# Kernel tuning notes

Measured on AMD Instinct MI355X. Metric: run time of the kernel, lower is better.

Reference implementation:

```python
import jax, jax.numpy as jnp
import numpy as np

B, N, E, D = 32, 512, 2048, 128
N_STEPS = 3


def setup_inputs() -> dict:
    key = jax.random.key(0)
    ks = jax.random.split(key, 16)
    s = 0.05
    return {
        "prop_state": jax.random.normal(ks[0], (B, N, D), jnp.float32),
        "edge_states": jax.random.normal(ks[1], (B, E, D), jnp.float32),
        "A": jax.random.uniform(ks[2], (B, N, E), jnp.float32) / E,
        "tem_features": jax.random.normal(ks[3], (B, 64), jnp.float32),
        "link_W": jax.random.normal(ks[4], (D, D), jnp.float32) * s,
        "link_b": jnp.zeros((D,), jnp.float32),
        "reset_W": jax.random.normal(ks[5], (2 * D, D), jnp.float32) * s,
        "reset_b": jnp.zeros((D,), jnp.float32),
        "update_W": jax.random.normal(ks[6], (2 * D, D), jnp.float32) * s,
        "update_b": jnp.zeros((D,), jnp.float32),
        "trans_W": jax.random.normal(ks[7], (2 * D, D), jnp.float32) * s,
        "trans_b": jnp.zeros((D,), jnp.float32),
        "att_W1": jax.random.normal(ks[8], (D, D), jnp.float32) * s,
        "att_b1": jnp.zeros((D,), jnp.float32),
        "att_W2": jax.random.normal(ks[9], (D, 1), jnp.float32) * s,
        "att_b2": jnp.zeros((1,), jnp.float32),
        "out_W": jax.random.normal(ks[10], (D, D), jnp.float32) * s,
        "out_b": jnp.zeros((D,), jnp.float32),
    }


def reference(prop_state, edge_states, A, tem_features,
              link_W, link_b, reset_W, reset_b, update_W, update_b,
              trans_W, trans_b, att_W1, att_b1, att_W2, att_b2, out_W, out_b):
    init_node = prop_state
    init_edge = edge_states
    for _ in range(N_STEPS):
        edge_states = edge_states @ link_W + link_b              # [B,E,D]
        a_cur = jnp.einsum('bne,bed->bnd', A, edge_states)       # [B,N,D]
        a = jnp.concatenate([a_cur, prop_state], axis=2)         # [B,N,2D]
        r = jax.nn.sigmoid(a @ reset_W + reset_b)
        z = jax.nn.sigmoid(a @ update_W + update_b)
        joined = jnp.concatenate([a_cur, r * prop_state], axis=2)
        h_hat = jnp.tanh(joined @ trans_W + trans_b)
        prop_state = (1.0 - z) * prop_state + z * h_hat
    # attention pooling
    atten = jnp.tanh(prop_state @ att_W1 + att_b1) @ att_W2 + att_b2   # [B,N,1]
    Aw = jax.nn.softmax(jnp.transpose(atten, (0, 2, 1)), axis=2)       # [B,1,N]
    out = jnp.tanh(prop_state @ out_W + out_b)                         # [B,N,D]
    mul = jnp.einsum('bqn,bnd->bqd', Aw, out)                          # [B,1,D]
    graph_out = jnp.tanh(jnp.squeeze(mul, axis=1))                     # [B,D]
    # residual block: mean over concatenated node+edge initial states
    feat = jnp.concatenate([init_node, init_edge], axis=1)             # [B,N+E,D]
    residual = jnp.mean(feat, axis=1)                                  # [B,D]
    res = jax.nn.relu(graph_out + residual)
    return res, mul, edge_states
```

## Files before the change

kernel.cpp:

```cpp
#include <hip/hip_runtime.h>
#include <hip/hip_bf16.h>


typedef unsigned short u16;
typedef __attribute__((ext_vector_type(4))) float f32x4;
typedef __attribute__((ext_vector_type(8))) short bf16x8;

#define DI static __device__ __forceinline__

DI u16 f2bf(float f) {
    unsigned u = __builtin_bit_cast(unsigned, f);
    return (u16)((u + 0x7fffu + ((u >> 16) & 1u)) >> 16);
}

DI bf16x8 cvt8(float4 a, float4 b) {
    u16 tmp[8] = {f2bf(a.x), f2bf(a.y), f2bf(a.z), f2bf(a.w),
                  f2bf(b.x), f2bf(b.y), f2bf(b.z), f2bf(b.w)};
    return *(const bf16x8*)tmp;
}

DI int imgIdx(int k, int n) {
    return (((k >> 5) * 128 + n) * 4 + (((k >> 3) & 3) ^ ((n >> 1) & 3))) * 8 + (k & 7);
}
DI bf16x8 wfragG(const u16* __restrict__ img, int kc, int tt, int l15, int quad) {
    return *(const bf16x8*)&img[(((kc * 128 + tt * 16 + l15) * 4) + (quad ^ ((l15 >> 1) & 3))) * 8];
}

#define MFMA16(a, b, c) __builtin_amdgcn_mfma_f32_16x16x32_bf16(a, b, c, 0, 0, 0)

__global__ __launch_bounds__(256) void k_prep1(
    const float* __restrict__ linkW, const float* __restrict__ resetW,
    const float* __restrict__ updateW, const float* __restrict__ transW,
    const float* __restrict__ attW1, const float* __restrict__ outW,
    float* __restrict__ W2, u16* __restrict__ linkImg, u16* __restrict__ WrImg,
    u16* __restrict__ WzImg, u16* __restrict__ WhImg, u16* __restrict__ attW1Img,
    u16* __restrict__ outWImg)
{
    int blk = blockIdx.x, t = threadIdx.x;
    if (blk < 256) {
        int idx = blk * 256 + t;
        int out = idx >> 2, q = idx & 3;
        int r = out >> 7, c = out & 127;
        const float* ar = linkW + r * 128 + q * 32;
        float acc = 0.f;
#pragma unroll
        for (int k = 0; k < 32; k++) acc += ar[k] * linkW[(q * 32 + k) * 128 + c];
        acc += __shfl_xor(acc, 1);
        acc += __shfl_xor(acc, 2);
        if (q == 0) W2[out] = acc;
    } else {
        const float* src; u16* dst; int base;
        if (blk < 260)      { src = resetW;  dst = WrImg;    base = 256; }
        else if (blk < 264) { src = updateW; dst = WzImg;    base = 260; }
        else if (blk < 268) { src = transW;  dst = WhImg;    base = 264; }
        else if (blk < 270) { src = linkW;   dst = linkImg;  base = 268; }
        else if (blk < 272) { src = attW1;   dst = attW1Img; base = 270; }
        else                { src = outW;    dst = outWImg;  base = 272; }
        int off = (blk - base) * 8192;
        for (int i = 0; i < 32; i++) {
            int e = off + t + i * 256;
            int k = e >> 7, n = e & 127;
            dst[imgIdx(k, n)] = f2bf(src[e]);
        }
    }
}

__global__ __launch_bounds__(256) void k_prep2(
    const float* __restrict__ linkW, const float* __restrict__ linkb,
    const float* __restrict__ W2, u16* __restrict__ W3Img, float* __restrict__ ebias)
{
    int blk = blockIdx.x, t = threadIdx.x;
    if (blk < 256) {
        int idx = blk * 256 + t;
        int out = idx >> 2, q = idx & 3;
        int r = out >> 7, c = out & 127;
        const float* ar = W2 + r * 128 + q * 32;
        float acc = 0.f;
#pragma unroll
        for (int k = 0; k < 32; k++) acc += ar[k] * linkW[(q * 32 + k) * 128 + c];
        acc += __shfl_xor(acc, 1);
        acc += __shfl_xor(acc, 2);
        if (q == 0) W3Img[imgIdx(r, c)] = f2bf(acc);
    } else if (t < 128) {
        float acc = linkb[t];
#pragma unroll 8
        for (int k = 0; k < 128; k++) acc += linkb[k] * (W2[k * 128 + t] + linkW[k * 128 + t]);
        ebias[t] = acc;
    }
}

__global__ __launch_bounds__(256) void k_te(
    const float* __restrict__ E0, u16* __restrict__ Eswz, float* __restrict__ resid)
{
    __shared__ alignas(16) u16 sT[4096];
    __shared__ float sCol[128];
    int t = threadIdx.x, kc = blockIdx.x, b = blockIdx.y;
    const float* Eb = E0 + (size_t)b * 262144 + (size_t)kc * 32 * 128;
    if (t < 128) sCol[t] = 0.f;
    float part[4] = {0.f, 0.f, 0.f, 0.f};
    int ncol = (t & 31) * 4;
    for (int i = 0; i < 4; i++) {
        int f4i = t + i * 256;
        int k5 = f4i >> 5;
        float4 v = *(const float4*)&Eb[k5 * 128 + ncol];
        int g = k5 >> 3, o = k5 & 7;
        float vv[4] = {v.x, v.y, v.z, v.w};
#pragma unroll
        for (int j = 0; j < 4; j++) {
            int n = ncol + j;
            sT[(n * 4 + (g ^ ((n >> 1) & 3))) * 8 + o] = f2bf(vv[j]);
            part[j] += vv[j];
        }
    }
    __syncthreads();
#pragma unroll
    for (int j = 0; j < 4; j++) atomicAdd(&sCol[ncol + j], part[j]);
    u16* dst = Eswz + (size_t)b * 262144 + (size_t)kc * 4096;
    ((uint4*)dst)[t] = ((const uint4*)sT)[t];
    ((uint4*)dst)[t + 256] = ((const uint4*)sT)[t + 256];
    __syncthreads();
    if (t < 128) atomicAdd(&resid[b * 128 + t], sCol[t]);
}

__global__ __launch_bounds__(256, 4) void k_main(
    const float* __restrict__ A, const u16* __restrict__ Eswz,
    const float* __restrict__ p0,
    const u16* __restrict__ linkImg, const u16* __restrict__ WrImg,
    const u16* __restrict__ WzImg, const u16* __restrict__ WhImg,
    const u16* __restrict__ attW1Img, const u16* __restrict__ outWImg,
    const float* __restrict__ link_b, const float* __restrict__ reset_b,
    const float* __restrict__ update_b, const float* __restrict__ trans_b,
    const float* __restrict__ att_b1, const float* __restrict__ att_W2,
    const float* __restrict__ att_b2, const float* __restrict__ out_b,
    float* __restrict__ atten, float* __restrict__ outPool,
    float* __restrict__ resid)
{
    __shared__ float sAcc2[2][16 * 65];
    __shared__ float sRs[2][16];
    __shared__ alignas(16) u16 sBuf[48 * 136];
    __shared__ float sRed[16];

    int t = threadIdx.x, wid = t >> 6, lane = t & 63, l15 = lane & 15, quad = lane >> 4;
    int tg = wid >> 1, kh = wid & 1;
    int bx = blockIdx.x;
    int g = bx >> 8, rmod = bx & 255;
    int b = (rmod & 7) + 8 * g;
    int s = (rmod >> 3) & 31;
    size_t r0 = (size_t)b * 512 + (size_t)s * 16;

    {
        const u16* Eb = Eswz + (size_t)b * 262144;
        const float* Ar = A + (r0 + l15) * 2048 + kh * 1024;

        f32x4 acc[4];
#pragma unroll
        for (int i = 0; i < 4; i++) acc[i] = (f32x4){0.f, 0.f, 0.f, 0.f};
        float rsum = 0.f;

        float4 xc = *(const float4*)&Ar[quad * 8];
        float4 yc = *(const float4*)&Ar[quad * 8 + 4];
        bf16x8 bc[4];
#pragma unroll
        for (int tt = 0; tt < 4; tt++) bc[tt] = wfragG(Eb, kh * 32, tg * 4 + tt, l15, quad);

        for (int kc = 0; kc < 32; kc++) {
            int kg = kh * 32 + kc;
            float4 xn, yn; bf16x8 bn[4];
            if (kc < 31) {
                xn = *(const float4*)&Ar[(kc + 1) * 32 + quad * 8];
                yn = *(const float4*)&Ar[(kc + 1) * 32 + quad * 8 + 4];
#pragma unroll
                for (int tt = 0; tt < 4; tt++) bn[tt] = wfragG(Eb, kg + 1, tg * 4 + tt, l15, quad);
            }
            rsum += xc.x + xc.y + xc.z + xc.w + yc.x + yc.y + yc.z + yc.w;
            bf16x8 af = cvt8(xc, yc);
#pragma unroll
            for (int tt = 0; tt < 4; tt++) acc[tt] = MFMA16(af, bc[tt], acc[tt]);
            if (kc < 31) {
                xc = xn; yc = yn;
#pragma unroll
                for (int tt = 0; tt < 4; tt++) bc[tt] = bn[tt];
            }
        }
        rsum += __shfl_xor(rsum, 16);
        rsum += __shfl_xor(rsum, 32);
        if (quad == 0 && tg == 0) sRs[kh][l15] = rsum;
        if (kh == 1) {
#pragma unroll
            for (int tt = 0; tt < 4; tt++)
#pragma unroll
                for (int r = 0; r < 4; r++)
                    sAcc2[tg][(quad * 4 + r) * 65 + tt * 16 + l15] = acc[tt][r];
        }
        if (t < 16) sRed[t] = 0.f;
        __syncthreads();
        if (kh == 0) {
#pragma unroll
            for (int tt = 0; tt < 4; tt++)
#pragma unroll
                for (int r = 0; r < 4; r++) {
                    float v = acc[tt][r] + sAcc2[tg][(quad * 4 + r) * 65 + tt * 16 + l15];
                    sBuf[(quad * 4 + r) * 136 + tg * 64 + tt * 16 + l15] = f2bf(v);
                }
        } else {
            int idx = tg * 64 + lane;
            int row = idx >> 3, c8 = (idx & 7) * 16;
            const float* pr = &p0[(r0 + row) * 128 + c8];
            float4 x0 = *(const float4*)&pr[0];
            float4 y0 = *(const float4*)&pr[4];
            float4 x1 = *(const float4*)&pr[8];
            float4 y1 = *(const float4*)&pr[12];
            *(bf16x8*)&sBuf[(16 + row) * 136 + c8] = cvt8(x0, y0);
            *(bf16x8*)&sBuf[(16 + row) * 136 + c8 + 8] = cvt8(x1, y1);
        }
    }
    __syncthreads();

    int ttA = wid * 2, ttB = wid * 2 + 1;
    int colA = ttA * 16 + l15, colB = ttB * 16 + l15;

    f32x4 pS[2];
#pragma unroll
    for (int j = 0; j < 2; j++)
#pragma unroll
        for (int r = 0; r < 4; r++)
            pS[j][r] = p0[(r0 + quad * 4 + r) * 128 + (wid * 2 + j) * 16 + l15];
    {
        float s0 = pS[0][0] + pS[0][1] + pS[0][2] + pS[0][3];
        float s1 = pS[1][0] + pS[1][1] + pS[1][2] + pS[1][3];
        s0 += __shfl_xor(s0, 16); s0 += __shfl_xor(s0, 32);
        s1 += __shfl_xor(s1, 16); s1 += __shfl_xor(s1, 32);
        if (quad == 0) {
            atomicAdd(&resid[b * 128 + colA], s0);
            atomicAdd(&resid[b * 128 + colB], s1);
        }
    }
    float sv[4];
#pragma unroll
    for (int r = 0; r < 4; r++) sv[r] = sRs[0][quad * 4 + r] + sRs[1][quad * 4 + r];
    float lbA = link_b[colA], lbB = link_b[colB];
    float rbA = reset_b[colA], rbB = reset_b[colB];
    float ubA = update_b[colA], ubB = update_b[colB];
    float tbA = trans_b[colA], tbB = trans_b[colB];

    f32x4 zero4 = {0.f, 0.f, 0.f, 0.f};
    int fcol = quad * 8;
    for (int step = 0; step < 3; step++) {
        f32x4 cA = zero4, cB = zero4;
#pragma unroll 2
        for (int kc = 0; kc < 4; kc++) {
            bf16x8 af = *(const bf16x8*)&sBuf[l15 * 136 + kc * 32 + fcol];
            cA = MFMA16(af, wfragG(linkImg, kc, ttA, l15, quad), cA);
            cB = MFMA16(af, wfragG(linkImg, kc, ttB, l15, quad), cB);
        }
        __syncthreads();
#pragma unroll
        for (int r = 0; r < 4; r++) {
            sBuf[(quad * 4 + r) * 136 + colA] = f2bf(cA[r] + sv[r] * lbA);
            sBuf[(quad * 4 + r) * 136 + colB] = f2bf(cB[r] + sv[r] * lbB);
        }
        __syncthreads();
        f32x4 rA = zero4, rB = zero4, zA = zero4, zB = zero4;
#pragma unroll 2
        for (int kc = 0; kc < 8; kc++) {
            int row = ((kc >> 2) * 16 + l15) * 136 + (kc & 3) * 32 + fcol;
            bf16x8 af = *(const bf16x8*)&sBuf[row];
            rA = MFMA16(af, wfragG(WrImg, kc, ttA, l15, quad), rA);
            rB = MFMA16(af, wfragG(WrImg, kc, ttB, l15, quad), rB);
            zA = MFMA16(af, wfragG(WzImg, kc, ttA, l15, quad), zA);
            zB = MFMA16(af, wfragG(WzImg, kc, ttB, l15, quad), zB);
        }
#pragma unroll
        for (int r = 0; r < 4; r++) {
            float rvA = 1.f / (1.f + __expf(-(rA[r] + rbA)));
            float rvB = 1.f / (1.f + __expf(-(rB[r] + rbB)));
            zA[r] = 1.f / (1.f + __expf(-(zA[r] + ubA)));
            zB[r] = 1.f / (1.f + __expf(-(zB[r] + ubB)));
            sBuf[(32 + quad * 4 + r) * 136 + colA] = f2bf(rvA * pS[0][r]);
            sBuf[(32 + quad * 4 + r) * 136 + colB] = f2bf(rvB * pS[1][r]);
        }
        __syncthreads();
        f32x4 hA = zero4, hB = zero4;
#pragma unroll 2
        for (int kc = 0; kc < 8; kc++) {
            int row = ((kc >> 2) * 32 + l15) * 136 + (kc & 3) * 32 + fcol;
            bf16x8 af = *(const bf16x8*)&sBuf[row];
            hA = MFMA16(af, wfragG(WhImg, kc, ttA, l15, quad), hA);
            hB = MFMA16(af, wfragG(WhImg, kc, ttB, l15, quad), hB);
        }
#pragma unroll
        for (int r = 0; r < 4; r++) {
            float h1 = tanhf(hA[r] + tbA), h2 = tanhf(hB[r] + tbB);
            pS[0][r] = (1.f - zA[r]) * pS[0][r] + zA[r] * h1;
            pS[1][r] = (1.f - zB[r]) * pS[1][r] + zB[r] * h2;
            sBuf[(16 + quad * 4 + r) * 136 + colA] = f2bf(pS[0][r]);
            sBuf[(16 + quad * 4 + r) * 136 + colB] = f2bf(pS[1][r]);
        }
        __syncthreads();
    }
    f32x4 atA = zero4, atB = zero4, oA = zero4, oB = zero4;
#pragma unroll 2
    for (int kc = 0; kc < 4; kc++) {
        bf16x8 pf = *(const bf16x8*)&sBuf[(16 + l15) * 136 + kc * 32 + fcol];
        atA = MFMA16(pf, wfragG(attW1Img, kc, ttA, l15, quad), atA);
        atB = MFMA16(pf, wfragG(attW1Img, kc, ttB, l15, quad), atB);
        oA  = MFMA16(pf, wfragG(outWImg,  kc, ttA, l15, quad), oA);
        oB  = MFMA16(pf, wfragG(outWImg,  kc, ttB, l15, quad), oB);
    }
    float b1A = att_b1[colA], b1B = att_b1[colB];
    float w2A = att_W2[colA], w2B = att_W2[colB];
    float obA = out_b[colA],  obB = out_b[colB];
    float pr[4];
#pragma unroll
    for (int r = 0; r < 4; r++) {
        pr[r] = tanhf(atA[r] + b1A) * w2A + tanhf(atB[r] + b1B) * w2B;
        outPool[(r0 + quad * 4 + r) * 128 + colA] = tanhf(oA[r] + obA);
        outPool[(r0 + quad * 4 + r) * 128 + colB] = tanhf(oB[r] + obB);
    }
#pragma unroll
    for (int r = 0; r < 4; r++) {
        float v = pr[r];
        v += __shfl_xor(v, 1); v += __shfl_xor(v, 2);
        v += __shfl_xor(v, 4); v += __shfl_xor(v, 8);
        if (l15 == 0) atomicAdd(&sRed[quad * 4 + r], v);
    }
    __syncthreads();
    if (t < 16) atten[r0 + t] = sRed[t] + att_b2[0];
}

__global__ __launch_bounds__(64) void k_eout(
    const float* __restrict__ E0, const u16* __restrict__ W3Img,
    const float* __restrict__ ebias, float* __restrict__ Eout)
{
    int t = threadIdx.x, l15 = t & 15, quad = t >> 4;
    size_t r0 = (size_t)blockIdx.x * 16;
    bf16x8 eF[4];
#pragma unroll
    for (int kc = 0; kc < 4; kc++) {
        float4 x = *(const float4*)&E0[(r0 + l15) * 128 + kc * 32 + quad * 8];
        float4 y = *(const float4*)&E0[(r0 + l15) * 128 + kc * 32 + quad * 8 + 4];
        eF[kc] = cvt8(x, y);
    }
    f32x4 acc[8];
#pragma unroll
    for (int i = 0; i < 8; i++) acc[i] = (f32x4){0.f, 0.f, 0.f, 0.f};
    {
        bf16x8 wc[8], wn[8];
#pragma unroll
        for (int tt = 0; tt < 8; tt++) wc[tt] = wfragG(W3Img, 0, tt, l15, quad);
#pragma unroll
        for (int kc = 0; kc < 4; kc++) {
            if (kc < 3)
#pragma unroll
                for (int tt = 0; tt < 8; tt++) wn[tt] = wfragG(W3Img, kc + 1, tt, l15, quad);
#pragma unroll
            for (int tt = 0; tt < 8; tt++) acc[tt] = MFMA16(eF[kc], wc[tt], acc[tt]);
            if (kc < 3)
#pragma unroll
                for (int tt = 0; tt < 8; tt++) wc[tt] = wn[tt];
        }
    }
#pragma unroll
    for (int tt = 0; tt < 8; tt++) {
        int col = tt * 16 + l15; float eb = ebias[col];
#pragma unroll
        for (int r = 0; r < 4; r++)
            Eout[(r0 + quad * 4 + r) * 128 + col] = acc[tt][r] + eb;
    }
}

__global__ __launch_bounds__(512) void k_fin(
    const float* __restrict__ atten, const float* __restrict__ outPool,
    const float* __restrict__ resid,
    float* __restrict__ outRes, float* __restrict__ outMul)
{
    __shared__ float swv[512];
    __shared__ float sred[512];
    __shared__ float sacc[4][128];
    int t = threadIdx.x, b = blockIdx.x;
    float a = atten[b * 512 + t];
    sred[t] = a; __syncthreads();
    for (int s = 256; s > 0; s >>= 1) { if (t < s) sred[t] = fmaxf(sred[t], sred[t + s]); __syncthreads(); }
    float mx = sred[0]; __syncthreads();
    float e = __expf(a - mx);
    swv[t] = e; sred[t] = e; __syncthreads();
    for (int s = 256; s > 0; s >>= 1) { if (t < s) sred[t] += sred[t + s]; __syncthreads(); }
    float Z = sred[0]; __syncthreads();
    int col = t & 127, q = t >> 7;
    const float* op = outPool + ((size_t)b * 512 + q * 128) * 128 + col;
    float accM = 0.f;
#pragma unroll 8
    for (int n = 0; n < 128; n++) accM += swv[q * 128 + n] * op[(size_t)n * 128];
    sacc[q][col] = accM;
    __syncthreads();
    if (t < 128) {
        float mulv = (sacc[0][t] + sacc[1][t] + sacc[2][t] + sacc[3][t]) / Z;
        float rv = resid[b * 128 + t] * (1.f / 2560.f);
        outMul[b * 128 + t] = mulv;
        outRes[b * 128 + t] = fmaxf(0.f, tanhf(mulv) + rv);
    }
}

extern "C" void kernel_launch(void* const* d_in, const int* in_sizes, int n_in,
                              void* d_out, int out_size, void* d_ws, size_t ws_size,
                              hipStream_t stream)
{
    const float* prop0  = (const float*)d_in[0];
    const float* edge0  = (const float*)d_in[1];
    const float* Amat   = (const float*)d_in[2];
    const float* linkW  = (const float*)d_in[4];
    const float* linkb  = (const float*)d_in[5];
    const float* resetW = (const float*)d_in[6];
    const float* resetb = (const float*)d_in[7];
    const float* updateW= (const float*)d_in[8];
    const float* updateb= (const float*)d_in[9];
    const float* transW = (const float*)d_in[10];
    const float* transb = (const float*)d_in[11];
    const float* attW1  = (const float*)d_in[12];
    const float* attb1  = (const float*)d_in[13];
    const float* attW2  = (const float*)d_in[14];
    const float* attb2  = (const float*)d_in[15];
    const float* outW   = (const float*)d_in[16];
    const float* outb   = (const float*)d_in[17];

    char* w = (char*)d_ws;
    float* ws_atten   = (float*)(w + 4259840);
    float* ws_resid   = (float*)(w + 4325376);
    float* ws_W2      = (float*)(w + 4341760);
    float* ws_ebias   = (float*)(w + 4407296);
    u16*   ws_linkImg = (u16*)(w + 4407808);
    u16*   ws_W3Img   = (u16*)(w + 4440576);
    u16*   ws_WrImg   = (u16*)(w + 4473344);
    u16*   ws_WzImg   = (u16*)(w + 4538880);
    u16*   ws_WhImg   = (u16*)(w + 4604416);
    u16*   ws_attW1Img= (u16*)(w + 4669952);
    u16*   ws_outWImg = (u16*)(w + 4702720);

    float* out_res  = (float*)d_out;
    float* out_mul  = out_res + 4096;
    float* out_edge = out_res + 8192;
    u16*   Eswz     = (u16*)out_edge;
    float* outPool  = out_edge + 4194304;

    hipMemsetAsync(ws_resid, 0, 32 * 128 * sizeof(float), stream);
    k_prep1<<<274, 256, 0, stream>>>(linkW, resetW, updateW, transW, attW1, outW,
                                     ws_W2, ws_linkImg, ws_WrImg, ws_WzImg, ws_WhImg,
                                     ws_attW1Img, ws_outWImg);
    k_prep2<<<257, 256, 0, stream>>>(linkW, linkb, ws_W2, ws_W3Img, ws_ebias);
    k_te<<<dim3(64, 32), 256, 0, stream>>>(edge0, Eswz, ws_resid);
    k_main<<<1024, 256, 0, stream>>>(Amat, Eswz, prop0,
                                     ws_linkImg, ws_WrImg, ws_WzImg, ws_WhImg,
                                     ws_attW1Img, ws_outWImg,
                                     linkb, resetb, updateb, transb,
                                     attb1, attW2, attb2, outb,
                                     ws_atten, outPool, ws_resid);
    k_fin<<<32, 512, 0, stream>>>(ws_atten, outPool, ws_resid, out_res, out_mul);
    k_eout<<<4096, 64, 0, stream>>>(edge0, ws_W3Img, ws_ebias, out_edge);
}
```

Baseline: 369.4 us.

## Process 32 rows per block in k_main and k_eout to reuse weight fragments

k_main now handles 32 node rows per block instead of 16, halving the grid to 512 blocks. Each loaded E/weight fragment feeds two MFMAs, which halves the global weight-fragment traffic per row across the A·E product and the GRU and pooling GEMMs. k_eout gets the same 32-row tiling, and k_fin uses 1024 threads to split the pooling reduction eight ways. The cost is more registers and LDS per block (launch bounds drop to 2 waves per SIMD) and fewer blocks to fill the GPU.

New measurement: 350.5 us. 1.05x faster.

```diff
diff --git a/kernel.cpp b/kernel.cpp
--- a/kernel.cpp
+++ b/kernel.cpp
@@ -122,7 +122,7 @@
     if (t < 128) atomicAdd(&resid[b * 128 + t], sCol[t]);
 }
 
-__global__ __launch_bounds__(256, 4) void k_main(
+__global__ __launch_bounds__(256, 2) void k_main(
     const float* __restrict__ A, const u16* __restrict__ Eswz,
     const float* __restrict__ p0,
     const u16* __restrict__ linkImg, const u16* __restrict__ WrImg,
@@ -135,83 +135,100 @@
     float* __restrict__ atten, float* __restrict__ outPool,
     float* __restrict__ resid)
 {
-    __shared__ float sAcc2[2][16 * 65];
-    __shared__ float sRs[2][16];
-    __shared__ alignas(16) u16 sBuf[48 * 136];
-    __shared__ float sRed[16];
+    __shared__ float sAcc2[2][2][16 * 65];
+    __shared__ float sRs[2][32];
+    __shared__ alignas(16) u16 sBuf[96 * 136];
+    __shared__ float sRed[32];
 
     int t = threadIdx.x, wid = t >> 6, lane = t & 63, l15 = lane & 15, quad = lane >> 4;
     int tg = wid >> 1, kh = wid & 1;
     int bx = blockIdx.x;
-    int g = bx >> 8, rmod = bx & 255;
+    int g = bx >> 7, rmod = bx & 127;
     int b = (rmod & 7) + 8 * g;
-    int s = (rmod >> 3) & 31;
-    size_t r0 = (size_t)b * 512 + (size_t)s * 16;
+    int s = (rmod >> 3) & 15;
+    size_t r0 = (size_t)b * 512 + (size_t)s * 32;
 
     {
         const u16* Eb = Eswz + (size_t)b * 262144;
-        const float* Ar = A + (r0 + l15) * 2048 + kh * 1024;
-
-        f32x4 acc[4];
-#pragma unroll
-        for (int i = 0; i < 4; i++) acc[i] = (f32x4){0.f, 0.f, 0.f, 0.f};
-        float rsum = 0.f;
-
-        float4 xc = *(const float4*)&Ar[quad * 8];
-        float4 yc = *(const float4*)&Ar[quad * 8 + 4];
+        const float* Ar0 = A + (r0 + l15) * 2048 + kh * 1024;
+        const float* Ar1 = A + (r0 + 16 + l15) * 2048 + kh * 1024;
+
+        f32x4 acc[2][4];
+#pragma unroll
+        for (int rg = 0; rg < 2; rg++)
+#pragma unroll
+            for (int i = 0; i < 4; i++) acc[rg][i] = (f32x4){0.f, 0.f, 0.f, 0.f};
+        float rs0 = 0.f, rs1 = 0.f;
+
+        float4 x0 = *(const float4*)&Ar0[quad * 8];
+        float4 y0 = *(const float4*)&Ar0[quad * 8 + 4];
+        float4 x1 = *(const float4*)&Ar1[quad * 8];
+        float4 y1 = *(const float4*)&Ar1[quad * 8 + 4];
+        rs0 += x0.x + x0.y + x0.z + x0.w + y0.x + y0.y + y0.z + y0.w;
+        rs1 += x1.x + x1.y + x1.z + x1.w + y1.x + y1.y + y1.z + y1.w;
+        bf16x8 aF0 = cvt8(x0, y0), aF1 = cvt8(x1, y1);
         bf16x8 bc[4];
 #pragma unroll
         for (int tt = 0; tt < 4; tt++) bc[tt] = wfragG(Eb, kh * 32, tg * 4 + tt, l15, quad);
 
         for (int kc = 0; kc < 32; kc++) {
-            int kg = kh * 32 + kc;
-            float4 xn, yn; bf16x8 bn[4];
+            float4 xn0, yn0, xn1, yn1; bf16x8 bn[4];
             if (kc < 31) {
-                xn = *(const float4*)&Ar[(kc + 1) * 32 + quad * 8];
-                yn = *(const float4*)&Ar[(kc + 1) * 32 + quad * 8 + 4];
-#pragma unroll
-                for (int tt = 0; tt < 4; tt++) bn[tt] = wfragG(Eb, kg + 1, tg * 4 + tt, l15, quad);
-            }
-            rsum += xc.x + xc.y + xc.z + xc.w + yc.x + yc.y + yc.z + yc.w;
-            bf16x8 af = cvt8(xc, yc);
-#pragma unroll
-            for (int tt = 0; tt < 4; tt++) acc[tt] = MFMA16(af, bc[tt], acc[tt]);
+                xn0 = *(const float4*)&Ar0[(kc + 1) * 32 + quad * 8];
+                yn0 = *(const float4*)&Ar0[(kc + 1) * 32 + quad * 8 + 4];
+                xn1 = *(const float4*)&Ar1[(kc + 1) * 32 + quad * 8];
+                yn1 = *(const float4*)&Ar1[(kc + 1) * 32 + quad * 8 + 4];
+#pragma unroll
+                for (int tt = 0; tt < 4; tt++)
+                    bn[tt] = wfragG(Eb, kh * 32 + kc + 1, tg * 4 + tt, l15, quad);
+            }
+#pragma unroll
+            for (int tt = 0; tt < 4; tt++) {
+                acc[0][tt] = MFMA16(aF0, bc[tt], acc[0][tt]);
+                acc[1][tt] = MFMA16(aF1, bc[tt], acc[1][tt]);
+            }
             if (kc < 31) {
-                xc = xn; yc = yn;
+                rs0 += xn0.x + xn0.y + xn0.z + xn0.w + yn0.x + yn0.y + yn0.z + yn0.w;
+                rs1 += xn1.x + xn1.y + xn1.z + xn1.w + yn1.x + yn1.y + yn1.z + yn1.w;
+                aF0 = cvt8(xn0, yn0); aF1 = cvt8(xn1, yn1);
 #pragma unroll
                 for (int tt = 0; tt < 4; tt++) bc[tt] = bn[tt];
             }
         }
-        rsum += __shfl_xor(rsum, 16);
-        rsum += __shfl_xor(rsum, 32);
-        if (quad == 0 && tg == 0) sRs[kh][l15] = rsum;
+        rs0 += __shfl_xor(rs0, 16); rs0 += __shfl_xor(rs0, 32);
+        rs1 += __shfl_xor(rs1, 16); rs1 += __shfl_xor(rs1, 32);
+        if (quad == 0 && tg == 0) { sRs[kh][l15] = rs0; sRs[kh][16 + l15] = rs1; }
         if (kh == 1) {
 #pragma unroll
-            for (int tt = 0; tt < 4; tt++)
-#pragma unroll
-                for (int r = 0; r < 4; r++)
-                    sAcc2[tg][(quad * 4 + r) * 65 + tt * 16 + l15] = acc[tt][r];
-        }
-        if (t < 16) sRed[t] = 0.f;
+            for (int rg = 0; rg < 2; rg++)
+#pragma unroll
+                for (int tt = 0; tt < 4; tt++)
+#pragma unroll
+                    for (int r = 0; r < 4; r++)
+                        sAcc2[tg][rg][(quad * 4 + r) * 65 + tt * 16 + l15] = acc[rg][tt][r];
+        }
+        if (t < 32) sRed[t] = 0.f;
         __syncthreads();
         if (kh == 0) {
 #pragma unroll
-            for (int tt = 0; tt < 4; tt++)
-#pragma unroll
-                for (int r = 0; r < 4; r++) {
-                    float v = acc[tt][r] + sAcc2[tg][(quad * 4 + r) * 65 + tt * 16 + l15];
-                    sBuf[(quad * 4 + r) * 136 + tg * 64 + tt * 16 + l15] = f2bf(v);
-                }
+            for (int rg = 0; rg < 2; rg++)
+#pragma unroll
+                for (int tt = 0; tt < 4; tt++)
+#pragma unroll
+                    for (int r = 0; r < 4; r++) {
+                        float v = acc[rg][tt][r] + sAcc2[tg][rg][(quad * 4 + r) * 65 + tt * 16 + l15];
+                        sBuf[(rg * 16 + quad * 4 + r) * 136 + tg * 64 + tt * 16 + l15] = f2bf(v);
+                    }
         } else {
             int idx = tg * 64 + lane;
-            int row = idx >> 3, c8 = (idx & 7) * 16;
-            const float* pr = &p0[(r0 + row) * 128 + c8];
-            float4 x0 = *(const float4*)&pr[0];
-            float4 y0 = *(const float4*)&pr[4];
-            float4 x1 = *(const float4*)&pr[8];
-            float4 y1 = *(const float4*)&pr[12];
-            *(bf16x8*)&sBuf[(16 + row) * 136 + c8] = cvt8(x0, y0);
-            *(bf16x8*)&sBuf[(16 + row) * 136 + c8 + 8] = cvt8(x1, y1);
+            int row = idx >> 2, cq = (idx & 3) * 32;
+            const float* pr = &p0[(r0 + row) * 128 + cq];
+#pragma unroll
+            for (int j = 0; j < 4; j++) {
+                float4 x = *(const float4*)&pr[j * 8];
+                float4 y = *(const float4*)&pr[j * 8 + 4];
+                *(bf16x8*)&sBuf[(32 + row) * 136 + cq + j * 8] = cvt8(x, y);
+            }
         }
     }
     __syncthreads();
@@ -219,15 +236,19 @@
     int ttA = wid * 2, ttB = wid * 2 + 1;
     int colA = ttA * 16 + l15, colB = ttB * 16 + l15;
 
-    f32x4 pS[2];
-#pragma unroll
-    for (int j = 0; j < 2; j++)
-#pragma unroll
-        for (int r = 0; r < 4; r++)
-            pS[j][r] = p0[(r0 + quad * 4 + r) * 128 + (wid * 2 + j) * 16 + l15];
+    f32x4 pS[2][2];
+#pragma unroll
+    for (int rg = 0; rg < 2; rg++)
+#pragma unroll
+        for (int j = 0; j < 2; j++)
+#pragma unroll
+            for (int r = 0; r < 4; r++)
+                pS[rg][j][r] = p0[(r0 + rg * 16 + quad * 4 + r) * 128 + (wid * 2 + j) * 16 + l15];
     {
-        float s0 = pS[0][0] + pS[0][1] + pS[0][2] + pS[0][3];
-        float s1 = pS[1][0] + pS[1][1] + pS[1][2] + pS[1][3];
+        float s0 = pS[0][0][0] + pS[0][0][1] + pS[0][0][2] + pS[0][0][3]
+                 + pS[1][0][0] + pS[1][0][1] + pS[1][0][2] + pS[1][0][3];
+        float s1 = pS[0][1][0] + pS[0][1][1] + pS[0][1][2] + pS[0][1][3]
+                 + pS[1][1][0] + pS[1][1][1] + pS[1][1][2] + pS[1][1][3];
         s0 += __shfl_xor(s0, 16); s0 += __shfl_xor(s0, 32);
         s1 += __shfl_xor(s1, 16); s1 += __shfl_xor(s1, 32);
         if (quad == 0) {
@@ -235,9 +256,12 @@
             atomicAdd(&resid[b * 128 + colB], s1);
         }
     }
-    float sv[4];
-#pragma unroll
-    for (int r = 0; r < 4; r++) sv[r] = sRs[0][quad * 4 + r] + sRs[1][quad * 4 + r];
+    float sv[2][4];
+#pragma unroll
+    for (int rg = 0; rg < 2; rg++)
+#pragma unroll
+        for (int r = 0; r < 4; r++)
+            sv[rg][r] = sRs[0][rg * 16 + quad * 4 + r] + sRs[1][rg * 16 + quad * 4 + r];
     float lbA = link_b[colA], lbB = link_b[colB];
     float rbA = reset_b[colA], rbB = reset_b[colB];
     float ubA = update_b[colA], ubB = update_b[colB];
@@ -246,86 +270,114 @@
     f32x4 zero4 = {0.f, 0.f, 0.f, 0.f};
     int fcol = quad * 8;
     for (int step = 0; step < 3; step++) {
-        f32x4 cA = zero4, cB = zero4;
-#pragma unroll 2
+        f32x4 cc[2][2];
+#pragma unroll
+        for (int rg = 0; rg < 2; rg++) { cc[rg][0] = zero4; cc[rg][1] = zero4; }
+#pragma unroll
         for (int kc = 0; kc < 4; kc++) {
-            bf16x8 af = *(const bf16x8*)&sBuf[l15 * 136 + kc * 32 + fcol];
-            cA = MFMA16(af, wfragG(linkImg, kc, ttA, l15, quad), cA);
-            cB = MFMA16(af, wfragG(linkImg, kc, ttB, l15, quad), cB);
+            bf16x8 wla = wfragG(linkImg, kc, ttA, l15, quad);
+            bf16x8 wlb = wfragG(linkImg, kc, ttB, l15, quad);
+            bf16x8 af0 = *(const bf16x8*)&sBuf[l15 * 136 + kc * 32 + fcol];
+            bf16x8 af1 = *(const bf16x8*)&sBuf[(16 + l15) * 136 + kc * 32 + fcol];
+            cc[0][0] = MFMA16(af0, wla, cc[0][0]); cc[0][1] = MFMA16(af0, wlb, cc[0][1]);
+            cc[1][0] = MFMA16(af1, wla, cc[1][0]); cc[1][1] = MFMA16(af1, wlb, cc[1][1]);
         }
         __syncthreads();
 #pragma unroll
-        for (int r = 0; r < 4; r++) {
-            sBuf[(quad * 4 + r) * 136 + colA] = f2bf(cA[r] + sv[r] * lbA);
-            sBuf[(quad * 4 + r) * 136 + colB] = f2bf(cB[r] + sv[r] * lbB);
-        }
+        for (int rg = 0; rg < 2; rg++)
+#pragma unroll
+            for (int r = 0; r < 4; r++) {
+                sBuf[(rg * 16 + quad * 4 + r) * 136 + colA] = f2bf(cc[rg][0][r] + sv[rg][r] * lbA);
+                sBuf[(rg * 16 + quad * 4 + r) * 136 + colB] = f2bf(cc[rg][1][r] + sv[rg][r] * lbB);
+            }
         __syncthreads();
-        f32x4 rA = zero4, rB = zero4, zA = zero4, zB = zero4;
-#pragma unroll 2
+        f32x4 rr[2][2], zz[2][2];
+#pragma unroll
+        for (int rg = 0; rg < 2; rg++) { rr[rg][0] = zero4; rr[rg][1] = zero4; zz[rg][0] = zero4; zz[rg][1] = zero4; }
+#pragma unroll 4
         for (int kc = 0; kc < 8; kc++) {
-            int row = ((kc >> 2) * 16 + l15) * 136 + (kc & 3) * 32 + fcol;
-            bf16x8 af = *(const bf16x8*)&sBuf[row];
-            rA = MFMA16(af, wfragG(WrImg, kc, ttA, l15, quad), rA);
-            rB = MFMA16(af, wfragG(WrImg, kc, ttB, l15, quad), rB);
-            zA = MFMA16(af, wfragG(WzImg, kc, ttA, l15, quad), zA);
-            zB = MFMA16(af, wfragG(WzImg, kc, ttB, l15, quad), zB);
-        }
-#pragma unroll
-        for (int r = 0; r < 4; r++) {
-            float rvA = 1.f / (1.f + __expf(-(rA[r] + rbA)));
-            float rvB = 1.f / (1.f + __expf(-(rB[r] + rbB)));
-            zA[r] = 1.f / (1.f + __expf(-(zA[r] + ubA)));
-            zB[r] = 1.f / (1.f + __expf(-(zB[r] + ubB)));
-            sBuf[(32 + quad * 4 + r) * 136 + colA] = f2bf(rvA * pS[0][r]);
-            sBuf[(32 + quad * 4 + r) * 136 + colB] = f2bf(rvB * pS[1][r]);
-        }
+            int base = (kc >> 2) * 32;
+            bf16x8 wra = wfragG(WrImg, kc, ttA, l15, quad);
+            bf16x8 wrb = wfragG(WrImg, kc, ttB, l15, quad);
+            bf16x8 wza = wfragG(WzImg, kc, ttA, l15, quad);
+            bf16x8 wzb = wfragG(WzImg, kc, ttB, l15, quad);
+            bf16x8 af0 = *(const bf16x8*)&sBuf[(base + l15) * 136 + (kc & 3) * 32 + fcol];
+            bf16x8 af1 = *(const bf16x8*)&sBuf[(base + 16 + l15) * 136 + (kc & 3) * 32 + fcol];
+            rr[0][0] = MFMA16(af0, wra, rr[0][0]); rr[0][1] = MFMA16(af0, wrb, rr[0][1]);
+            zz[0][0] = MFMA16(af0, wza, zz[0][0]); zz[0][1] = MFMA16(af0, wzb, zz[0][1]);
+            rr[1][0] = MFMA16(af1, wra, rr[1][0]); rr[1][1] = MFMA16(af1, wrb, rr[1][1]);
+            zz[1][0] = MFMA16(af1, wza, zz[1][0]); zz[1][1] = MFMA16(af1, wzb, zz[1][1]);
+        }
+#pragma unroll
+        for (int rg = 0; rg < 2; rg++)
+#pragma unroll
+            for (int r = 0; r < 4; r++) {
+                float rvA = 1.f / (1.f + __expf(-(rr[rg][0][r] + rbA)));
+                float rvB = 1.f / (1.f + __expf(-(rr[rg][1][r] + rbB)));
+                zz[rg][0][r] = 1.f / (1.f + __expf(-(zz[rg][0][r] + ubA)));
+                zz[rg][1][r] = 1.f / (1.f + __expf(-(zz[rg][1][r] + ubB)));
+                sBuf[(64 + rg * 16 + quad * 4 + r) * 136 + colA] = f2bf(rvA * pS[rg][0][r]);
+                sBuf[(64 + rg * 16 + quad * 4 + r) * 136 + colB] = f2bf(rvB * pS[rg][1][r]);
+            }
         __syncthreads();
-        f32x4 hA = zero4, hB = zero4;
-#pragma unroll 2
+        f32x4 hh[2][2];
+#pragma unroll
+        for (int rg = 0; rg < 2; rg++) { hh[rg][0] = zero4; hh[rg][1] = zero4; }
+#pragma unroll 4
         for (int kc = 0; kc < 8; kc++) {
-            int row = ((kc >> 2) * 32 + l15) * 136 + (kc & 3) * 32 + fcol;
-            bf16x8 af = *(const bf16x8*)&sBuf[row];
-            hA = MFMA16(af, wfragG(WhImg, kc, ttA, l15, quad), hA);
-            hB = MFMA16(af, wfragG(WhImg, kc, ttB, l15, quad), hB);
-        }
-#pragma unroll
-        for (int r = 0; r < 4; r++) {
-            float h1 = tanhf(hA[r] + tbA), h2 = tanhf(hB[r] + tbB);
-            pS[0][r] = (1.f - zA[r]) * pS[0][r] + zA[r] * h1;
-            pS[1][r] = (1.f - zB[r]) * pS[1][r] + zB[r] * h2;
-            sBuf[(16 + quad * 4 + r) * 136 + colA] = f2bf(pS[0][r]);
-            sBuf[(16 + quad * 4 + r) * 136 + colB] = f2bf(pS[1][r]);
-        }
+            int base = (kc >> 2) * 64;
+            bf16x8 wha = wfragG(WhImg, kc, ttA, l15, quad);
+            bf16x8 whb = wfragG(WhImg, kc, ttB, l15, quad);
+            bf16x8 af0 = *(const bf16x8*)&sBuf[(base + l15) * 136 + (kc & 3) * 32 + fcol];
+            bf16x8 af1 = *(const bf16x8*)&sBuf[(base + 16 + l15) * 136 + (kc & 3) * 32 + fcol];
+            hh[0][0] = MFMA16(af0, wha, hh[0][0]); hh[0][1] = MFMA16(af0, whb, hh[0][1]);
+            hh[1][0] = MFMA16(af1, wha, hh[1][0]); hh[1][1] = MFMA16(af1, whb, hh[1][1]);
+        }
+#pragma unroll
+        for (int rg = 0; rg < 2; rg++)
+#pragma unroll
+            for (int r = 0; r < 4; r++) {
+                float h1 = tanhf(hh[rg][0][r] + tbA), h2 = tanhf(hh[rg][1][r] + tbB);
+                pS[rg][0][r] = (1.f - zz[rg][0][r]) * pS[rg][0][r] + zz[rg][0][r] * h1;
+                pS[rg][1][r] = (1.f - zz[rg][1][r]) * pS[rg][1][r] + zz[rg][1][r] * h2;
+                sBuf[(32 + rg * 16 + quad * 4 + r) * 136 + colA] = f2bf(pS[rg][0][r]);
+                sBuf[(32 + rg * 16 + quad * 4 + r) * 136 + colB] = f2bf(pS[rg][1][r]);
+            }
         __syncthreads();
     }
-    f32x4 atA = zero4, atB = zero4, oA = zero4, oB = zero4;
-#pragma unroll 2
+    f32x4 at[2][2], oo[2][2];
+#pragma unroll
+    for (int rg = 0; rg < 2; rg++) { at[rg][0] = zero4; at[rg][1] = zero4; oo[rg][0] = zero4; oo[rg][1] = zero4; }
+#pragma unroll
     for (int kc = 0; kc < 4; kc++) {
-        bf16x8 pf = *(const bf16x8*)&sBuf[(16 + l15) * 136 + kc * 32 + fcol];
-        atA = MFMA16(pf, wfragG(attW1Img, kc, ttA, l15, quad), atA);
-        atB = MFMA16(pf, wfragG(attW1Img, kc, ttB, l15, quad), atB);
-        oA  = MFMA16(pf, wfragG(outWImg,  kc, ttA, l15, quad), oA);
-        oB  = MFMA16(pf, wfragG(outWImg,  kc, ttB, l15, quad), oB);
+        bf16x8 wa  = wfragG(attW1Img, kc, ttA, l15, quad);
+        bf16x8 wb  = wfragG(attW1Img, kc, ttB, l15, quad);
+        bf16x8 woa = wfragG(outWImg,  kc, ttA, l15, quad);
+        bf16x8 wob = wfragG(outWImg,  kc, ttB, l15, quad);
+        bf16x8 pf0 = *(const bf16x8*)&sBuf[(32 + l15) * 136 + kc * 32 + fcol];
+        bf16x8 pf1 = *(const bf16x8*)&sBuf[(48 + l15) * 136 + kc * 32 + fcol];
+        at[0][0] = MFMA16(pf0, wa, at[0][0]);  at[0][1] = MFMA16(pf0, wb, at[0][1]);
+        oo[0][0] = MFMA16(pf0, woa, oo[0][0]); oo[0][1] = MFMA16(pf0, wob, oo[0][1]);
+        at[1][0] = MFMA16(pf1, wa, at[1][0]);  at[1][1] = MFMA16(pf1, wb, at[1][1]);
+        oo[1][0] = MFMA16(pf1, woa, oo[1][0]); oo[1][1] = MFMA16(pf1, wob, oo[1][1]);
     }
     float b1A = att_b1[colA], b1B = att_b1[colB];
     float w2A = att_W2[colA], w2B = att_W2[colB];
     float obA = out_b[colA],  obB = out_b[colB];
-    float pr[4];
-#pragma unroll
-    for (int r = 0; r < 4; r++) {
-        pr[r] = tanhf(atA[r] + b1A) * w2A + tanhf(atB[r] + b1B) * w2B;
-        outPool[(r0 + quad * 4 + r) * 128 + colA] = tanhf(oA[r] + obA);
-        outPool[(r0 + quad * 4 + r) * 128 + colB] = tanhf(oB[r] + obB);
-    }
-#pragma unroll
-    for (int r = 0; r < 4; r++) {
-        float v = pr[r];
-        v += __shfl_xor(v, 1); v += __shfl_xor(v, 2);
-        v += __shfl_xor(v, 4); v += __shfl_xor(v, 8);
-        if (l15 == 0) atomicAdd(&sRed[quad * 4 + r], v);
-    }
-    __syncthreads();
-    if (t < 16) atten[r0 + t] = sRed[t] + att_b2[0];
+#pragma unroll
+    for (int rg = 0; rg < 2; rg++)
+#pragma unroll
+        for (int r = 0; r < 4; r++) {
+            float pr = tanhf(at[rg][0][r] + b1A) * w2A + tanhf(at[rg][1][r] + b1B) * w2B;
+            outPool[(r0 + rg * 16 + quad * 4 + r) * 128 + colA] = tanhf(oo[rg][0][r] + obA);
+            outPool[(r0 + rg * 16 + quad * 4 + r) * 128 + colB] = tanhf(oo[rg][1][r] + obB);
+            float v = pr;
+            v += __shfl_xor(v, 1); v += __shfl_xor(v, 2);
+            v += __shfl_xor(v, 4); v += __shfl_xor(v, 8);
+            if (l15 == 0) atomicAdd(&sRed[rg * 16 + quad * 4 + r], v);
+        }
+    __syncthreads();
+    if (t < 32) atten[r0 + t] = sRed[t] + att_b2[0];
 }
 
 __global__ __launch_bounds__(64) void k_eout(
@@ -333,17 +385,20 @@
     const float* __restrict__ ebias, float* __restrict__ Eout)
 {
     int t = threadIdx.x, l15 = t & 15, quad = t >> 4;
-    size_t r0 = (size_t)blockIdx.x * 16;
-    bf16x8 eF[4];
-#pragma unroll
-    for (int kc = 0; kc < 4; kc++) {
-        float4 x = *(const float4*)&E0[(r0 + l15) * 128 + kc * 32 + quad * 8];
-        float4 y = *(const float4*)&E0[(r0 + l15) * 128 + kc * 32 + quad * 8 + 4];
-        eF[kc] = cvt8(x, y);
-    }
-    f32x4 acc[8];
-#pragma unroll
-    for (int i = 0; i < 8; i++) acc[i] = (f32x4){0.f, 0.f, 0.f, 0.f};
+    size_t r0 = (size_t)blockIdx.x * 32;
+    bf16x8 eF[2][4];
+#pragma unroll
+    for (int rg = 0; rg < 2; rg++)
+#pragma unroll
+        for (int kc = 0; kc < 4; kc++) {
+            const float* er = &E0[(r0 + rg * 16 + l15) * 128 + kc * 32 + quad * 8];
+            eF[rg][kc] = cvt8(*(const float4*)er, *(const float4*)(er + 4));
+        }
+    f32x4 acc[2][8];
+#pragma unroll
+    for (int rg = 0; rg < 2; rg++)
+#pragma unroll
+        for (int i = 0; i < 8; i++) acc[rg][i] = (f32x4){0.f, 0.f, 0.f, 0.f};
     {
         bf16x8 wc[8], wn[8];
 #pragma unroll
@@ -354,7 +409,10 @@
 #pragma unroll
                 for (int tt = 0; tt < 8; tt++) wn[tt] = wfragG(W3Img, kc + 1, tt, l15, quad);
 #pragma unroll
-            for (int tt = 0; tt < 8; tt++) acc[tt] = MFMA16(eF[kc], wc[tt], acc[tt]);
+            for (int tt = 0; tt < 8; tt++) {
+                acc[0][tt] = MFMA16(eF[0][kc], wc[tt], acc[0][tt]);
+                acc[1][tt] = MFMA16(eF[1][kc], wc[tt], acc[1][tt]);
+            }
             if (kc < 3)
 #pragma unroll
                 for (int tt = 0; tt < 8; tt++) wc[tt] = wn[tt];
@@ -364,37 +422,41 @@
     for (int tt = 0; tt < 8; tt++) {
         int col = tt * 16 + l15; float eb = ebias[col];
 #pragma unroll
-        for (int r = 0; r < 4; r++)
-            Eout[(r0 + quad * 4 + r) * 128 + col] = acc[tt][r] + eb;
-    }
-}
-
-__global__ __launch_bounds__(512) void k_fin(
+        for (int rg = 0; rg < 2; rg++)
+#pragma unroll
+            for (int r = 0; r < 4; r++)
+                Eout[(r0 + rg * 16 + quad * 4 + r) * 128 + col] = acc[rg][tt][r] + eb;
+    }
+}
+
+__global__ __launch_bounds__(1024) void k_fin(
     const float* __restrict__ atten, const float* __restrict__ outPool,
     const float* __restrict__ resid,
     float* __restrict__ outRes, float* __restrict__ outMul)
 {
     __shared__ float swv[512];
     __shared__ float sred[512];
-    __shared__ float sacc[4][128];
+    __shared__ float sacc[8][128];
     int t = threadIdx.x, b = blockIdx.x;
-    float a = atten[b * 512 + t];
-    sred[t] = a; __syncthreads();
+    float a = 0.f;
+    if (t < 512) { a = atten[b * 512 + t]; sred[t] = a; }
+    __syncthreads();
     for (int s = 256; s > 0; s >>= 1) { if (t < s) sred[t] = fmaxf(sred[t], sred[t + s]); __syncthreads(); }
     float mx = sred[0]; __syncthreads();
-    float e = __expf(a - mx);
-    swv[t] = e; sred[t] = e; __syncthreads();
+    if (t < 512) { float e = __expf(a - mx); swv[t] = e; sred[t] = e; }
+    __syncthreads();
     for (int s = 256; s > 0; s >>= 1) { if (t < s) sred[t] += sred[t + s]; __syncthreads(); }
     float Z = sred[0]; __syncthreads();
     int col = t & 127, q = t >> 7;
-    const float* op = outPool + ((size_t)b * 512 + q * 128) * 128 + col;
+    const float* op = outPool + ((size_t)b * 512 + q * 64) * 128 + col;
     float accM = 0.f;
 #pragma unroll 8
-    for (int n = 0; n < 128; n++) accM += swv[q * 128 + n] * op[(size_t)n * 128];
+    for (int n = 0; n < 64; n++) accM += swv[q * 64 + n] * op[(size_t)n * 128];
     sacc[q][col] = accM;
     __syncthreads();
     if (t < 128) {
-        float mulv = (sacc[0][t] + sacc[1][t] + sacc[2][t] + sacc[3][t]) / Z;
+        float mulv = (sacc[0][t] + sacc[1][t] + sacc[2][t] + sacc[3][t] +
+                      sacc[4][t] + sacc[5][t] + sacc[6][t] + sacc[7][t]) / Z;
         float rv = resid[b * 128 + t] * (1.f / 2560.f);
         outMul[b * 128 + t] = mulv;
         outRes[b * 128 + t] = fmaxf(0.f, tanhf(mulv) + rv);
@@ -448,12 +510,12 @@
                                      ws_attW1Img, ws_outWImg);
     k_prep2<<<257, 256, 0, stream>>>(linkW, linkb, ws_W2, ws_W3Img, ws_ebias);
     k_te<<<dim3(64, 32), 256, 0, stream>>>(edge0, Eswz, ws_resid);
-    k_main<<<1024, 256, 0, stream>>>(Amat, Eswz, prop0,
-                                     ws_linkImg, ws_WrImg, ws_WzImg, ws_WhImg,
-                                     ws_attW1Img, ws_outWImg,
-                                     linkb, resetb, updateb, transb,
-                                     attb1, attW2, attb2, outb,
-                                     ws_atten, outPool, ws_resid);
-    k_fin<<<32, 512, 0, stream>>>(ws_atten, outPool, ws_resid, out_res, out_mul);
-    k_eout<<<4096, 64, 0, stream>>>(edge0, ws_W3Img, ws_ebias, out_edge);
-}
+    k_main<<<512, 256, 0, stream>>>(Amat, Eswz, prop0,
+                                    ws_linkImg, ws_WrImg, ws_WzImg, ws_WhImg,
+                                    ws_attW1Img, ws_outWImg,
+                                    linkb, resetb, updateb, transb,
+                                    attb1, attW2, attb2, outb,
+                                    ws_atten, outPool, ws_resid);
+    k_fin<<<32, 1024, 0, stream>>>(ws_atten, outPool, ws_resid, out_res, out_mul);
+    k_eout<<<2048, 64, 0, stream>>>(edge0, ws_W3Img, ws_ebias, out_edge);
+}
```
